# Kernel tuning notes

Measured on AMD Instinct MI355X. Metric: run time of the kernel, lower is better.

## Reference

```python
import jax, jax.numpy as jnp
import numpy as np

INPUT_SIZE = 256
NUM_LABELS = 50
L = NUM_LABELS + 1  # internal label count incl. pad label (index L-1)
B, T = 64, 256


def setup_inputs() -> dict:
    key = jax.random.key(0)
    k = jax.random.split(key, 8)
    inp = {
        "input": jax.random.normal(k[0], (B, T, INPUT_SIZE), dtype=jnp.float32),
        "mask": jnp.ones((B, T), dtype=jnp.float32),
        "target": jax.random.randint(k[1], (B, T), 0, NUM_LABELS),
        # state_nn: Linear(input_size, L)
        "state_W": jax.random.normal(k[2], (INPUT_SIZE, L), dtype=jnp.float32) * 0.05,
        "state_b": jnp.zeros((L,), dtype=jnp.float32),
        # trans_nn: Linear(input_size, L*L) (bigram=True)
        "trans_W": jax.random.normal(k[3], (INPUT_SIZE, L * L), dtype=jnp.float32) * 0.05,
        "trans_b": jnp.zeros((L * L,), dtype=jnp.float32),
    }
    return inp


def _energy(x, mask, state_W, state_b, trans_W, trans_b):
    # out_s: [B,T,L]  (unary scores), out_t: [B,T,L,L] (bigram transitions)
    out_s = jnp.einsum("bti,il->btl", x, state_W) + state_b
    out_t = (jnp.einsum("bti,io->bto", x, trans_W) + trans_b).reshape(
        x.shape[0], x.shape[1], L, L
    )
    energy = out_t + out_s[:, :, None, :]  # [B,T,L,L]
    return energy * mask[:, :, None, None]


def reference(input, mask, target, state_W, state_b, trans_W, trans_b):
    """ChainCRF.loss: -log p(target | input) per batch element, shape [B]."""
    energy = _energy(input, mask, state_W, state_b, trans_W, trans_b)
    e_t = jnp.transpose(energy, (1, 0, 2, 3))  # [T,B,L,L]
    tgt_t = target.T                            # [T,B]
    msk_t = mask.T                              # [T,B]
    bidx = jnp.arange(input.shape[0])

    # t = 0: start from pad label (index L-1)
    partition0 = e_t[0][:, L - 1, :]                       # [B,L]
    tgt0 = e_t[0][bidx, L - 1, tgt_t[0]]                   # [B]

    def step(carry, xs):
        part, tgt_e, prev = carry
        curr, tgt, m = xs  # curr [B,L,L], tgt [B], m [B]
        part_new = jax.nn.logsumexp(curr + part[:, :, None], axis=1)
        part = part + (part_new - part) * m[:, None]
        tgt_e = tgt_e + curr[bidx, prev, tgt]
        return (part, tgt_e, tgt), None

    (part, tgt_e, _), _ = jax.lax.scan(
        step, (partition0, tgt0, tgt_t[0]), (e_t[1:], tgt_t[1:], msk_t[1:])
    )
    return jax.nn.logsumexp(part, axis=1) - tgt_e
```

## Files before the change

kernel.cpp:

```cpp
#include <hip/hip_runtime.h>
#include <hip/hip_bf16.h>

#define B_    64
#define T_    256
#define K_    256
#define L_    51
#define LL_   2601
#define RS_   64
#define NG_   3328
#define PST_  4096
#define MT_   128
#define NT_   128
#define TS_   72

typedef __bf16 bf16x8 __attribute__((ext_vector_type(8)));
typedef float  f32x4  __attribute__((ext_vector_type(4)));
typedef unsigned int u32x4 __attribute__((ext_vector_type(4)));
typedef u32x4 __attribute__((may_alias)) u32x4_a;
typedef unsigned long long ull;
typedef ull __attribute__((may_alias)) ull_a;

static __device__ __forceinline__ bf16x8 as_bf16x8(u32x4 u) {
    return __builtin_bit_cast(bf16x8, u);
}
static __device__ __forceinline__ unsigned short bf16bits(float x) {
    return __builtin_bit_cast(unsigned short, __float2bfloat16(x));
}
static __device__ __forceinline__ ull pack4(f32x4 a) {
    return (ull)bf16bits(a[0]) | ((ull)bf16bits(a[1]) << 16) |
           ((ull)bf16bits(a[2]) << 32) | ((ull)bf16bits(a[3]) << 48);
}
static __device__ __forceinline__ void gld_lds16(const void* g, void* l) {
    __builtin_amdgcn_global_load_lds(
        (const __attribute__((address_space(1))) unsigned int*)g,
        (__attribute__((address_space(3))) unsigned int*)l, 16, 0, 0);
}

#define DPP_STEP(v, OP, CTRL)                                                   \
    {                                                                           \
        int _x = __builtin_bit_cast(int, v);                                    \
        float _o = __builtin_bit_cast(                                          \
            float, __builtin_amdgcn_update_dpp(_x, _x, CTRL, 0xF, 0xF, true));  \
        v = OP(v, _o);                                                          \
    }
static __device__ __forceinline__ float addf(float a, float b) { return a + b; }

__global__ __launch_bounds__(256) void prep_w(
    const float* __restrict__ trans_W, const float* __restrict__ trans_b,
    const float* __restrict__ state_W, const float* __restrict__ state_b,
    __hip_bfloat16* __restrict__ Wt, float* __restrict__ bias)
{
    const int n  = blockIdx.x * 64 + (threadIdx.x >> 2);
    const int kq = (threadIdx.x & 3) * 64;
    const int j  = n >> 6;
    const int i  = n & 63;
    const bool valid = (i < L_) && (j < L_);
    const int o = i * L_ + j;

    __hip_bfloat16 tmp[64];
#pragma unroll
    for (int kk = 0; kk < 64; ++kk) {
        const int k = kq + kk;
        float w = valid ? (trans_W[(size_t)k * LL_ + o] + state_W[k * L_ + j]) : 0.f;
        tmp[kk] = __float2bfloat16(w);
    }
    u32x4* dst = (u32x4*)(Wt + (size_t)n * K_ + kq);
    const u32x4* src = (const u32x4*)tmp;
#pragma unroll
    for (int q = 0; q < 8; ++q) dst[q] = src[q];

    if ((threadIdx.x & 3) == 0)
        bias[n] = valid ? (trans_b[o] + state_b[j]) : 0.f;
}

__global__ void prep_x(const float4* __restrict__ x4, ushort4* __restrict__ xb4, int n4)
{
    for (int idx = blockIdx.x * blockDim.x + threadIdx.x; idx < n4;
         idx += gridDim.x * blockDim.x) {
        float4 v = x4[idx];
        ushort4 o;
        o.x = bf16bits(v.x); o.y = bf16bits(v.y);
        o.z = bf16bits(v.z); o.w = bf16bits(v.w);
        xb4[idx] = o;
    }
}

__global__ void zero_pad(u32x4* __restrict__ P16, int nBT)
{
    const int per = (PST_ - NG_) / 8;
    const int tot = nBT * per;
    const u32x4 z = {};
    for (int idx = blockIdx.x * blockDim.x + threadIdx.x; idx < tot;
         idx += gridDim.x * blockDim.x) {
        const int m = idx / per;
        const int q = idx - m * per;
        P16[(size_t)m * (PST_ / 8) + (NG_ / 8) + q] = z;
    }
}

__global__ __launch_bounds__(256) void gemm_energy(
    const __hip_bfloat16* __restrict__ xb,
    const __hip_bfloat16* __restrict__ Wt,
    const float* __restrict__ bias,
    const float* __restrict__ mask,
    __hip_bfloat16* __restrict__ P,
    int t0, int Tc, int TcShift)
{
    __shared__ __align__(16) __hip_bfloat16 As[MT_ * 128];
    __shared__ __align__(16) __hip_bfloat16 Bs[NT_ * 128];

    const int tid  = threadIdx.x;
    const int lane = tid & 63;
    const int wv   = tid >> 6;
    const int quad = lane >> 4;
    const int l16  = lane & 15;
    const int m0 = blockIdx.y * MT_;
    const int n0 = blockIdx.x * NT_;
    const int mrow0 = (wv >> 1) * 64;
    const int ncol0 = (wv & 1) * 64;

    const int srow = wv * 4 + (lane >> 4);
    const int spos = lane & 15;

    f32x4 acc[4][4] = {};

    for (int kp = 0; kp < 2; ++kp) {
        if (kp) __syncthreads();
#pragma unroll
        for (int it = 0; it < 8; ++it) {
            const int r  = it * 16 + srow;
            const int kc = spos ^ (r & 15);
            const int ma = m0 + r;
            const int rg = (ma >> TcShift) * T_ + t0 + (ma & (Tc - 1));
            gld_lds16((const char*)xb + (size_t)rg * 512 + kp * 256 + kc * 16,
                      (char*)As + it * 4096 + wv * 1024);
            gld_lds16((const char*)Wt + (size_t)(n0 + r) * 512 + kp * 256 + kc * 16,
                      (char*)Bs + it * 4096 + wv * 1024);
        }
        asm volatile("s_waitcnt vmcnt(0)" ::: "memory");
        __syncthreads();

        const u32x4_a* Av = (const u32x4_a*)As;
        const u32x4_a* Bv = (const u32x4_a*)Bs;
#pragma unroll
        for (int kk = 0; kk < 4; ++kk) {
            bf16x8 af[4], bfr[4];
#pragma unroll
            for (int f = 0; f < 4; ++f) {
                const int ra = mrow0 + f * 16 + l16;
                af[f]  = as_bf16x8(Av[ra * 16 + ((kk * 4 + quad) ^ (ra & 15))]);
                const int rb = ncol0 + f * 16 + l16;
                bfr[f] = as_bf16x8(Bv[rb * 16 + ((kk * 4 + quad) ^ (rb & 15))]);
            }
#pragma unroll
            for (int nf = 0; nf < 4; ++nf)
#pragma unroll
                for (int mf = 0; mf < 4; ++mf)
                    acc[nf][mf] = __builtin_amdgcn_mfma_f32_16x16x32_bf16(
                        bfr[nf], af[mf], acc[nf][mf], 0, 0, 0);
        }
    }

    const int jcol = (n0 + ncol0) >> 6;
    const bool jok = jcol < L_;
#pragma unroll
    for (int mf = 0; mf < 4; ++mf) {
        const int m  = m0 + mrow0 + mf * 16 + l16;
        const int bb = m >> TcShift;
        const int tl = m & (Tc - 1);
        const int t  = t0 + tl;
        const float mval = mask[bb * T_ + t];
        const bool idm = (mval == 0.f) && (t != 0);
        __hip_bfloat16* prow = P + (size_t)m * PST_;
#pragma unroll
        for (int nf = 0; nf < 4; ++nf) {
            const int nbase = n0 + ncol0 + nf * 16 + quad * 4;
            const int ibase = nf * 16 + quad * 4;
            const f32x4 bv = *(const f32x4*)(bias + nbase);
            ull pk = 0;
#pragma unroll
            for (int r = 0; r < 4; ++r) {
                const int i = ibase + r;
                const bool ok = jok && (i < L_);
                float v;
                if (idm) v = (ok && i == jcol) ? 1.f : 0.f;
                else     v = ok ? __expf((acc[nf][mf][r] + bv[r]) * mval) : 0.f;
                pk |= (ull)bf16bits(v) << (16 * r);
            }
            *(ull_a*)(prow + nbase) = pk;
        }
    }
}

__global__ __launch_bounds__(256) void prod_quad(
    const __hip_bfloat16* __restrict__ P,
    __hip_bfloat16* __restrict__ Q,
    int Tc)
{
    __shared__ u32x4 Sm[4][512];
    __shared__ __align__(16) unsigned short T1t[64 * TS_];
    __shared__ __align__(16) unsigned short T3t[64 * TS_];
    __shared__ __align__(16) unsigned short W2t[64 * TS_];
    __shared__ __align__(16) unsigned short W4b[64 * TS_];

    const int tid  = threadIdx.x;
    const int wv   = tid >> 6;
    const int lane = tid & 63;
    const int quad = lane >> 4;
    const int l16  = lane & 15;
    const int bq = blockIdx.x;
    const int Tq = Tc >> 2;
    const int b  = bq / Tq;
    const int tq = bq - b * Tq;
    const __hip_bfloat16* tile0 = P + (size_t)(b * Tc + tq * 4) * PST_;

#pragma unroll
    for (int q = 0; q < 8; ++q) {
        const int idx  = q * 4 + wv;
        const int tile = idx >> 3;
        const int part = idx & 7;
        const int slot = part * 64 + lane;
        const int r    = slot >> 3;
        const int csrc = (slot & 7) ^ (r & 7);
        gld_lds16((const char*)(tile0 + (size_t)tile * PST_) + (r * 8 + csrc) * 16,
                  (char*)&Sm[tile][part * 64]);
    }

    u32x4 idf[2];
    {
        const int e = l16 & 7;
        const unsigned int bits = (e & 1) ? 0x3F800000u : 0x3F80u;
#pragma unroll
        for (int par = 0; par < 2; ++par) {
            u32x4 v = {};
            if (quad == (l16 >> 3) + par * 2) v[e >> 1] = bits;
            idf[par] = v;
        }
    }

    const int ra = wv * 16 + l16;
    const f32x4 z = {};
    asm volatile("s_waitcnt vmcnt(0)" ::: "memory");
    __syncthreads();

#pragma unroll
    for (int tt = 0; tt < 2; ++tt) {
        const u32x4* S = Sm[tt * 2];
        bf16x8 a0 = as_bf16x8(S[ra * 8 + (quad ^ (ra & 7))]);
        bf16x8 a1 = as_bf16x8(S[ra * 8 + ((4 + quad) ^ (ra & 7))]);
        unsigned short* dst = tt ? T3t : T1t;
#pragma unroll
        for (int nf = 0; nf < 4; ++nf) {
            f32x4 d = __builtin_amdgcn_mfma_f32_16x16x32_bf16(
                (nf >> 1) ? a1 : a0, as_bf16x8(idf[nf & 1]), z, 0, 0, 0);
            *(ull_a*)(dst + (nf * 16 + l16) * TS_ + wv * 16 + quad * 4) = pack4(d);
        }
    }
    __syncthreads();

    {
        bf16x8 a2[2], a3[2];
#pragma unroll
        for (int ks = 0; ks < 2; ++ks) {
            a2[ks] = as_bf16x8(Sm[1][ra * 8 + ((ks * 4 + quad) ^ (ra & 7))]);
            a3[ks] = as_bf16x8(*(const u32x4_a*)(T3t + ra * TS_ + ks * 32 + quad * 8));
        }
#pragma unroll
        for (int nf = 0; nf < 4; ++nf) {
            const int rb = nf * 16 + l16;
            f32x4 u = z, v = z;
#pragma unroll
            for (int ks = 0; ks < 2; ++ks) {
                bf16x8 bU = as_bf16x8(*(const u32x4_a*)(T1t + rb * TS_ + ks * 32 + quad * 8));
                bf16x8 bV = as_bf16x8(Sm[3][rb * 8 + ((ks * 4 + quad) ^ (rb & 7))]);
                u = __builtin_amdgcn_mfma_f32_16x16x32_bf16(a2[ks], bU, u, 0, 0, 0);
                v = __builtin_amdgcn_mfma_f32_16x16x32_bf16(a3[ks], bV, v, 0, 0, 0);
            }
            *(ull_a*)(W2t + rb * TS_ + wv * 16 + quad * 4) = pack4(u);
            *(ull_a*)(W4b + rb * TS_ + wv * 16 + quad * 4) = pack4(v);
        }
    }
    __syncthreads();

    {
        bf16x8 aw[2];
#pragma unroll
        for (int ks = 0; ks < 2; ++ks)
            aw[ks] = as_bf16x8(*(const u32x4_a*)(W2t + ra * TS_ + ks * 32 + quad * 8));
#pragma unroll
        for (int nf = 0; nf < 4; ++nf) {
            const int rb = nf * 16 + l16;
            f32x4 d = z;
#pragma unroll
            for (int ks = 0; ks < 2; ++ks) {
                bf16x8 bw = as_bf16x8(*(const u32x4_a*)(W4b + rb * TS_ + ks * 32 + quad * 8));
                d = __builtin_amdgcn_mfma_f32_16x16x32_bf16(aw[ks], bw, d, 0, 0, 0);
            }
            *(ull_a*)(T1t + rb * TS_ + wv * 16 + quad * 4) = pack4(d);
        }
    }
    __syncthreads();

    u32x4* qout = (u32x4*)(Q + (size_t)bq * PST_);
#pragma unroll
    for (int c = tid; c < 512; c += 256) {
        const int row = c >> 3;
        const int pos = c & 7;
        qout[row * 8 + pos] = *(const u32x4_a*)(T1t + row * TS_ + pos * 8);
    }
}

__global__ __launch_bounds__(64) void tgt_kernel(
    const __hip_bfloat16* __restrict__ P, const int* __restrict__ target,
    const float* __restrict__ mask, float* __restrict__ tgt_ws, int t0, int Tc)
{
    const int b = blockIdx.x, lane = threadIdx.x;
    float s = 0.f;
    for (int tl = lane; tl < Tc; tl += 64) {
        const int t = t0 + tl;
        const int j = target[b * T_ + t];
        const int i = (t == 0) ? (L_ - 1) : target[b * T_ + t - 1];
        const float m = (t == 0) ? 1.f : mask[b * T_ + t];
        if (m != 0.f) {
            const float pval = __bfloat162float(P[(size_t)(b * Tc + tl) * PST_ + j * RS_ + i]);
            s += __logf(pval);
        }
    }
#pragma unroll
    for (int d = 1; d < 64; d <<= 1) s += __shfl_xor(s, d);
    if (lane == 0) {
        if (t0 == 0) tgt_ws[b] = s;
        else         tgt_ws[b] += s;
    }
}

__global__ __launch_bounds__(64, 1) void scan_q(
    const __hip_bfloat16* __restrict__ Q,
    float* __restrict__ p_ws, float* __restrict__ ls_ws,
    const float* __restrict__ tgt_ws, float* __restrict__ out,
    int t0q, int Tq, int Tqtot)
{
    __shared__ __align__(16) unsigned short p_arr[64];

    const int b    = blockIdx.x;
    const int lane = threadIdx.x;
    const int quad = lane >> 4;
    const int l16  = lane & 15;

    float pv[4] = {0.f, 0.f, 0.f, 0.f};
    float logscale = 0.f;
    if (t0q == 0) {
        p_arr[lane] = (lane == L_ - 1) ? (unsigned short)0x3F80 : (unsigned short)0;
    } else {
#pragma unroll
        for (int f = 0; f < 4; ++f) pv[f] = p_ws[b * 64 + f * 16 + l16];
        logscale = ls_ws[b];
        p_arr[quad * 16 + l16] = bf16bits(pv[quad]);
    }
    asm volatile("s_waitcnt lgkmcnt(0)" ::: "memory");

    int off[8];
#pragma unroll
    for (int f = 0; f < 4; ++f)
#pragma unroll
        for (int ks = 0; ks < 2; ++ks)
            off[f * 2 + ks] = (f * 16 + l16) * 8 + ks * 4 + quad;

    const u32x4* gp = (const u32x4*)Q + (size_t)b * Tq * (PST_ / 8);
    const u32x4_a* pa = (const u32x4_a*)p_arr;

    u32x4 s0[8], s1[8], s2[8], s3[8];
    auto fetch = [&](u32x4 (&st)[8], int tl) {
        const u32x4* g = gp + (size_t)tl * (PST_ / 8);
#pragma unroll
        for (int q = 0; q < 8; ++q) st[q] = g[off[q]];
    };
    fetch(s0, 0);
    if (1 < Tq) fetch(s1, 1);
    if (2 < Tq) fetch(s2, 2);
    if (3 < Tq) fetch(s3, 3);

    auto step = [&](u32x4 (&st)[8], int tl) {
        bf16x8 a0 = as_bf16x8(pa[quad]);
        bf16x8 a1 = as_bf16x8(pa[4 + quad]);
        const f32x4 z = {};
        f32x4 ae[4], ao[4];
#pragma unroll
        for (int f = 0; f < 4; ++f) {
            ae[f] = __builtin_amdgcn_mfma_f32_16x16x32_bf16(a0, as_bf16x8(st[f * 2 + 0]), z, 0, 0, 0);
            ao[f] = __builtin_amdgcn_mfma_f32_16x16x32_bf16(a1, as_bf16x8(st[f * 2 + 1]), z, 0, 0, 0);
        }
#pragma unroll
        for (int f = 0; f < 4; ++f) pv[f] = ae[f][0] + ao[f][0];

        if (((tl & 1) == 1) || (tl == Tq - 1)) {
            float mx = fmaxf(fmaxf(pv[0], pv[1]), fmaxf(pv[2], pv[3]));
            DPP_STEP(mx, fmaxf, 0xB1);
            DPP_STEP(mx, fmaxf, 0x4E);
            DPP_STEP(mx, fmaxf, 0x124);
            DPP_STEP(mx, fmaxf, 0x128);
            const float inv = 1.f / mx;
            logscale += __logf(mx);
#pragma unroll
            for (int f = 0; f < 4; ++f) pv[f] *= inv;
        }
        p_arr[quad * 16 + l16] = bf16bits(pv[quad]);
        asm volatile("s_waitcnt lgkmcnt(0)" ::: "memory");
    };

    for (int tl = 0; tl < Tq; tl += 4) {
        step(s0, tl);
        if (tl + 4 < Tq) fetch(s0, tl + 4);
        if (tl + 1 < Tq) { step(s1, tl + 1); if (tl + 5 < Tq) fetch(s1, tl + 5); }
        if (tl + 2 < Tq) { step(s2, tl + 2); if (tl + 6 < Tq) fetch(s2, tl + 6); }
        if (tl + 3 < Tq) { step(s3, tl + 3); if (tl + 7 < Tq) fetch(s3, tl + 7); }
    }

    if (t0q + Tq == Tqtot) {
        float s = pv[0] + pv[1] + pv[2] + pv[3];
        DPP_STEP(s, addf, 0xB1);
        DPP_STEP(s, addf, 0x4E);
        DPP_STEP(s, addf, 0x124);
        DPP_STEP(s, addf, 0x128);
        if (lane == 0) out[b] = logscale + __logf(s) - tgt_ws[b];
    } else {
        if (quad == 0) {
#pragma unroll
            for (int f = 0; f < 4; ++f) p_ws[b * 64 + f * 16 + l16] = pv[f];
        }
        if (lane == 0) ls_ws[b] = logscale;
    }
}

extern "C" void kernel_launch(void* const* d_in, const int* in_sizes, int n_in,
                              void* d_out, int out_size, void* d_ws, size_t ws_size,
                              hipStream_t stream)
{
    (void)in_sizes; (void)n_in; (void)out_size;
    const float* x       = (const float*)d_in[0];
    const float* mask    = (const float*)d_in[1];
    const int*   target  = (const int*)d_in[2];
    const float* state_W = (const float*)d_in[3];
    const float* state_b = (const float*)d_in[4];
    const float* trans_W = (const float*)d_in[5];
    const float* trans_b = (const float*)d_in[6];
    float* out = (float*)d_out;

    char* ws = (char*)d_ws;
    size_t off = 0;
    auto alloc = [&](size_t bytes) -> void* {
        void* p = ws + off;
        off = (off + bytes + 255) & ~(size_t)255;
        return p;
    };

    __hip_bfloat16* Wt   = (__hip_bfloat16*)alloc((size_t)NG_ * K_ * 2);
    float*          bias = (float*)alloc((size_t)NG_ * 4);
    __hip_bfloat16* xb   = (__hip_bfloat16*)alloc((size_t)B_ * T_ * K_ * 2);
    float*          p_ws = (float*)alloc((size_t)B_ * 64 * 4);
    float*          ls   = (float*)alloc((size_t)B_ * 4);
    float*          tgte = (float*)alloc((size_t)B_ * 4);
    const size_t fixed = off;

    int Tc = 256;
    while (Tc > 4 && fixed + (size_t)Tc * B_ * PST_ * 2 * 5 / 4 + 512 > ws_size) Tc >>= 1;
    __hip_bfloat16* P = (__hip_bfloat16*)alloc((size_t)Tc * B_ * PST_ * 2);
    __hip_bfloat16* Q = (__hip_bfloat16*)alloc((size_t)(Tc / 4) * B_ * PST_ * 2);
    int TcShift = 0;
    while ((1 << TcShift) < Tc) ++TcShift;

    prep_w<<<dim3(NG_ / 64), 256, 0, stream>>>(trans_W, trans_b, state_W, state_b, Wt, bias);
    prep_x<<<dim3(2048), 256, 0, stream>>>((const float4*)x, (ushort4*)xb, B_ * T_ * K_ / 4);
    zero_pad<<<dim3(2048), 256, 0, stream>>>((u32x4*)P, B_ * Tc);

    for (int t0 = 0; t0 < T_; t0 += Tc) {
        gemm_energy<<<dim3(NG_ / NT_, (B_ * Tc) / MT_), 256, 0, stream>>>(
            xb, Wt, bias, mask, P, t0, Tc, TcShift);
        prod_quad<<<dim3(B_ * (Tc / 4)), 256, 0, stream>>>(P, Q, Tc);
        tgt_kernel<<<dim3(B_), 64, 0, stream>>>(P, target, mask, tgte, t0, Tc);
        scan_q<<<dim3(B_), 64, 0, stream>>>(Q, p_ws, ls, tgte, out,
                                            t0 / 4, Tc / 4, T_ / 4);
    }
}
```

Baseline: 229.8 us.

## Fuse prep kernels, stage GEMM epilogue through LDS, merge target into scan

Merges the weight-transpose, x-to-bf16 conversion and pad-zeroing kernels into one launch, and rewrites the weight transpose to go through shared memory so global accesses are coalesced. The GEMM epilogue now writes its bf16 tile to LDS first, then stores full 16-byte rows to P instead of scattered 8-byte writes. The target-score kernel is folded into scan_q as a second wave that runs alongside the scan. Together these remove launches and uncoalesced traffic, at the cost of an extra LDS round trip and two extra barriers in the GEMM.

After: 213.9 us. 6.9% less time.

```diff
diff --git a/kernel.cpp b/kernel.cpp
--- a/kernel.cpp
+++ b/kernel.cpp
@@ -12,6 +12,7 @@
 #define MT_   128
 #define NT_   128
 #define TS_   72
+#define ES_   136
 
 typedef __bf16 bf16x8 __attribute__((ext_vector_type(8)));
 typedef float  f32x4  __attribute__((ext_vector_type(4)));
@@ -45,56 +46,70 @@
     }
 static __device__ __forceinline__ float addf(float a, float b) { return a + b; }
 
-__global__ __launch_bounds__(256) void prep_w(
+__global__ __launch_bounds__(256) void prep_all(
     const float* __restrict__ trans_W, const float* __restrict__ trans_b,
     const float* __restrict__ state_W, const float* __restrict__ state_b,
-    __hip_bfloat16* __restrict__ Wt, float* __restrict__ bias)
+    const float* __restrict__ x,
+    __hip_bfloat16* __restrict__ Wt, float* __restrict__ bias,
+    __hip_bfloat16* __restrict__ xb, __hip_bfloat16* __restrict__ P, int Tc)
 {
-    const int n  = blockIdx.x * 64 + (threadIdx.x >> 2);
-    const int kq = (threadIdx.x & 3) * 64;
-    const int j  = n >> 6;
-    const int i  = n & 63;
-    const bool valid = (i < L_) && (j < L_);
-    const int o = i * L_ + j;
-
-    __hip_bfloat16 tmp[64];
-#pragma unroll
-    for (int kk = 0; kk < 64; ++kk) {
-        const int k = kq + kk;
-        float w = valid ? (trans_W[(size_t)k * LL_ + o] + state_W[k * L_ + j]) : 0.f;
-        tmp[kk] = __float2bfloat16(w);
-    }
-    u32x4* dst = (u32x4*)(Wt + (size_t)n * K_ + kq);
-    const u32x4* src = (const u32x4*)tmp;
-#pragma unroll
-    for (int q = 0; q < 8; ++q) dst[q] = src[q];
-
-    if ((threadIdx.x & 3) == 0)
-        bias[n] = valid ? (trans_b[o] + state_b[j]) : 0.f;
-}
-
-__global__ void prep_x(const float4* __restrict__ x4, ushort4* __restrict__ xb4, int n4)
-{
-    for (int idx = blockIdx.x * blockDim.x + threadIdx.x; idx < n4;
-         idx += gridDim.x * blockDim.x) {
-        float4 v = x4[idx];
-        ushort4 o;
-        o.x = bf16bits(v.x); o.y = bf16bits(v.y);
-        o.z = bf16bits(v.z); o.w = bf16bits(v.w);
-        xb4[idx] = o;
-    }
-}
-
-__global__ void zero_pad(u32x4* __restrict__ P16, int nBT)
-{
-    const int per = (PST_ - NG_) / 8;
-    const int tot = nBT * per;
-    const u32x4 z = {};
-    for (int idx = blockIdx.x * blockDim.x + threadIdx.x; idx < tot;
-         idx += gridDim.x * blockDim.x) {
-        const int m = idx / per;
-        const int q = idx - m * per;
-        P16[(size_t)m * (PST_ / 8) + (NG_ / 8) + q] = z;
+    __shared__ __align__(16) __hip_bfloat16 Wl[52 * 258];
+    const int blk = blockIdx.x, tid = threadIdx.x;
+
+    if (blk < 64) {
+        const int i = blk;
+        if (i < L_) {
+            const int jp = tid & 63, kk = tid >> 6;
+            if (jp < 52) {
+                for (int k = kk; k < K_; k += 4) {
+                    float v = 0.f;
+                    if (jp < L_) v = trans_W[(size_t)k * LL_ + i * L_ + jp] +
+                                     state_W[k * L_ + jp];
+                    Wl[jp * 258 + k] = __float2bfloat16(v);
+                }
+            }
+            __syncthreads();
+            for (int idx = tid; idx < 52 * 32; idx += 256) {
+                const int j = idx >> 5, c = idx & 31;
+                const unsigned int* row = (const unsigned int*)&Wl[j * 258];
+                u32x4 v;
+                v[0] = row[c * 4 + 0]; v[1] = row[c * 4 + 1];
+                v[2] = row[c * 4 + 2]; v[3] = row[c * 4 + 3];
+                *(u32x4*)(Wt + (size_t)((j << 6) + i) * K_ + c * 8) = v;
+            }
+        } else {
+            const u32x4 z = {};
+            for (int idx = tid; idx < 52 * 32; idx += 256) {
+                const int j = idx >> 5, c = idx & 31;
+                *(u32x4*)(Wt + (size_t)((j << 6) + i) * K_ + c * 8) = z;
+            }
+        }
+        if (tid < 52) {
+            const int j = tid;
+            bias[(j << 6) + i] =
+                (i < L_ && j < L_) ? trans_b[i * L_ + j] + state_b[j] : 0.f;
+        }
+    } else if (blk < 64 + 1024) {
+        const int n4 = B_ * T_ * K_ / 4;
+        const float4* x4 = (const float4*)x;
+        ushort4* xb4 = (ushort4*)xb;
+        for (int idx = (blk - 64) * 256 + tid; idx < n4; idx += 1024 * 256) {
+            float4 v = x4[idx];
+            ushort4 o;
+            o.x = bf16bits(v.x); o.y = bf16bits(v.y);
+            o.z = bf16bits(v.z); o.w = bf16bits(v.w);
+            xb4[idx] = o;
+        }
+    } else {
+        const int per = (PST_ - NG_) / 8;
+        const int tot = B_ * Tc * per;
+        u32x4* P16 = (u32x4*)P;
+        const u32x4 z = {};
+        for (int idx = (blk - 1088) * 256 + tid; idx < tot; idx += 1024 * 256) {
+            const int m = idx / per;
+            const int q = idx - m * per;
+            P16[(size_t)m * (PST_ / 8) + (NG_ / 8) + q] = z;
+        }
     }
 }
 
@@ -106,8 +121,9 @@
     __hip_bfloat16* __restrict__ P,
     int t0, int Tc, int TcShift)
 {
-    __shared__ __align__(16) __hip_bfloat16 As[MT_ * 128];
-    __shared__ __align__(16) __hip_bfloat16 Bs[NT_ * 128];
+    __shared__ __align__(16) __hip_bfloat16 SH[2 * MT_ * 128];
+    __hip_bfloat16* As = SH;
+    __hip_bfloat16* Bs = SH + MT_ * 128;
 
     const int tid  = threadIdx.x;
     const int lane = tid & 63;
@@ -160,35 +176,45 @@
                         bfr[nf], af[mf], acc[nf][mf], 0, 0, 0);
         }
     }
-
+    __syncthreads();
+
+    unsigned short* E = (unsigned short*)SH;
     const int jcol = (n0 + ncol0) >> 6;
     const bool jok = jcol < L_;
 #pragma unroll
     for (int mf = 0; mf < 4; ++mf) {
-        const int m  = m0 + mrow0 + mf * 16 + l16;
+        const int ml = mrow0 + mf * 16 + l16;
+        const int m  = m0 + ml;
         const int bb = m >> TcShift;
         const int tl = m & (Tc - 1);
         const int t  = t0 + tl;
         const float mval = mask[bb * T_ + t];
         const bool idm = (mval == 0.f) && (t != 0);
-        __hip_bfloat16* prow = P + (size_t)m * PST_;
 #pragma unroll
         for (int nf = 0; nf < 4; ++nf) {
-            const int nbase = n0 + ncol0 + nf * 16 + quad * 4;
-            const int ibase = nf * 16 + quad * 4;
-            const f32x4 bv = *(const f32x4*)(bias + nbase);
+            const int nl = ncol0 + nf * 16 + quad * 4;
+            const f32x4 bv = *(const f32x4*)(bias + n0 + nl);
             ull pk = 0;
 #pragma unroll
             for (int r = 0; r < 4; ++r) {
-                const int i = ibase + r;
+                const int i = (nl + r) & 63;
                 const bool ok = jok && (i < L_);
                 float v;
                 if (idm) v = (ok && i == jcol) ? 1.f : 0.f;
                 else     v = ok ? __expf((acc[nf][mf][r] + bv[r]) * mval) : 0.f;
                 pk |= (ull)bf16bits(v) << (16 * r);
             }
-            *(ull_a*)(prow + nbase) = pk;
-        }
+            *(ull_a*)(E + ml * ES_ + nl) = pk;
+        }
+    }
+    __syncthreads();
+
+#pragma unroll
+    for (int it2 = 0; it2 < 8; ++it2) {
+        const int idx = it2 * 256 + tid;
+        const int ml = idx >> 4, c = idx & 15;
+        const u32x4 v = *(const u32x4_a*)(E + ml * ES_ + c * 8);
+        *(u32x4*)(P + (size_t)(m0 + ml) * PST_ + n0 + c * 8) = v;
     }
 }
 
@@ -310,125 +336,133 @@
     }
 }
 
-__global__ __launch_bounds__(64) void tgt_kernel(
-    const __hip_bfloat16* __restrict__ P, const int* __restrict__ target,
-    const float* __restrict__ mask, float* __restrict__ tgt_ws, int t0, int Tc)
-{
-    const int b = blockIdx.x, lane = threadIdx.x;
-    float s = 0.f;
-    for (int tl = lane; tl < Tc; tl += 64) {
-        const int t = t0 + tl;
-        const int j = target[b * T_ + t];
-        const int i = (t == 0) ? (L_ - 1) : target[b * T_ + t - 1];
-        const float m = (t == 0) ? 1.f : mask[b * T_ + t];
-        if (m != 0.f) {
-            const float pval = __bfloat162float(P[(size_t)(b * Tc + tl) * PST_ + j * RS_ + i]);
-            s += __logf(pval);
-        }
-    }
-#pragma unroll
-    for (int d = 1; d < 64; d <<= 1) s += __shfl_xor(s, d);
-    if (lane == 0) {
-        if (t0 == 0) tgt_ws[b] = s;
-        else         tgt_ws[b] += s;
-    }
-}
-
-__global__ __launch_bounds__(64, 1) void scan_q(
+__global__ __launch_bounds__(128, 1) void scan_q(
     const __hip_bfloat16* __restrict__ Q,
+    const __hip_bfloat16* __restrict__ P,
+    const int* __restrict__ target, const float* __restrict__ mask,
     float* __restrict__ p_ws, float* __restrict__ ls_ws,
-    const float* __restrict__ tgt_ws, float* __restrict__ out,
+    float* __restrict__ tgt_ws, float* __restrict__ out,
     int t0q, int Tq, int Tqtot)
 {
     __shared__ __align__(16) unsigned short p_arr[64];
+    __shared__ float tgt_sh;
 
     const int b    = blockIdx.x;
-    const int lane = threadIdx.x;
+    const int tid  = threadIdx.x;
+    const int wv   = tid >> 6;
+    const int lane = tid & 63;
     const int quad = lane >> 4;
     const int l16  = lane & 15;
+    const int t0 = t0q << 2, Tc = Tq << 2;
 
     float pv[4] = {0.f, 0.f, 0.f, 0.f};
     float logscale = 0.f;
-    if (t0q == 0) {
-        p_arr[lane] = (lane == L_ - 1) ? (unsigned short)0x3F80 : (unsigned short)0;
+
+    if (wv == 0) {
+        if (t0q == 0) {
+            p_arr[lane] = (lane == L_ - 1) ? (unsigned short)0x3F80 : (unsigned short)0;
+        } else {
+#pragma unroll
+            for (int f = 0; f < 4; ++f) pv[f] = p_ws[b * 64 + f * 16 + l16];
+            logscale = ls_ws[b];
+            p_arr[quad * 16 + l16] = bf16bits(pv[quad]);
+        }
+        asm volatile("s_waitcnt lgkmcnt(0)" ::: "memory");
+
+        int off[8];
+#pragma unroll
+        for (int f = 0; f < 4; ++f)
+#pragma unroll
+            for (int ks = 0; ks < 2; ++ks)
+                off[f * 2 + ks] = (f * 16 + l16) * 8 + ks * 4 + quad;
+
+        const u32x4* gp = (const u32x4*)Q + (size_t)b * Tq * (PST_ / 8);
+        const u32x4_a* pa = (const u32x4_a*)p_arr;
+
+        u32x4 s0[8], s1[8], s2[8], s3[8];
+        auto fetch = [&](u32x4 (&st)[8], int tl) {
+            const u32x4* g = gp + (size_t)tl * (PST_ / 8);
+#pragma unroll
+            for (int q = 0; q < 8; ++q) st[q] = g[off[q]];
+        };
+        fetch(s0, 0);
+        if (1 < Tq) fetch(s1, 1);
+        if (2 < Tq) fetch(s2, 2);
+        if (3 < Tq) fetch(s3, 3);
+
+        auto step = [&](u32x4 (&st)[8], int tl) {
+            bf16x8 a0 = as_bf16x8(pa[quad]);
+            bf16x8 a1 = as_bf16x8(pa[4 + quad]);
+            const f32x4 z = {};
+            f32x4 ae[4], ao[4];
+#pragma unroll
+            for (int f = 0; f < 4; ++f) {
+                ae[f] = __builtin_amdgcn_mfma_f32_16x16x32_bf16(a0, as_bf16x8(st[f * 2 + 0]), z, 0, 0, 0);
+                ao[f] = __builtin_amdgcn_mfma_f32_16x16x32_bf16(a1, as_bf16x8(st[f * 2 + 1]), z, 0, 0, 0);
+            }
+#pragma unroll
+            for (int f = 0; f < 4; ++f) pv[f] = ae[f][0] + ao[f][0];
+
+            if (((tl & 1) == 1) || (tl == Tq - 1)) {
+                float mx = fmaxf(fmaxf(pv[0], pv[1]), fmaxf(pv[2], pv[3]));
+                DPP_STEP(mx, fmaxf, 0xB1);
+                DPP_STEP(mx, fmaxf, 0x4E);
+                DPP_STEP(mx, fmaxf, 0x124);
+                DPP_STEP(mx, fmaxf, 0x128);
+                const float inv = 1.f / mx;
+                logscale += __logf(mx);
+#pragma unroll
+                for (int f = 0; f < 4; ++f) pv[f] *= inv;
+            }
+            p_arr[quad * 16 + l16] = bf16bits(pv[quad]);
+            asm volatile("s_waitcnt lgkmcnt(0)" ::: "memory");
+        };
+
+        for (int tl = 0; tl < Tq; tl += 4) {
+            step(s0, tl);
+            if (tl + 4 < Tq) fetch(s0, tl + 4);
+            if (tl + 1 < Tq) { step(s1, tl + 1); if (tl + 5 < Tq) fetch(s1, tl + 5); }
+            if (tl + 2 < Tq) { step(s2, tl + 2); if (tl + 6 < Tq) fetch(s2, tl + 6); }
+            if (tl + 3 < Tq) { step(s3, tl + 3); if (tl + 7 < Tq) fetch(s3, tl + 7); }
+        }
     } else {
-#pragma unroll
-        for (int f = 0; f < 4; ++f) pv[f] = p_ws[b * 64 + f * 16 + l16];
-        logscale = ls_ws[b];
-        p_arr[quad * 16 + l16] = bf16bits(pv[quad]);
-    }
-    asm volatile("s_waitcnt lgkmcnt(0)" ::: "memory");
-
-    int off[8];
-#pragma unroll
-    for (int f = 0; f < 4; ++f)
-#pragma unroll
-        for (int ks = 0; ks < 2; ++ks)
-            off[f * 2 + ks] = (f * 16 + l16) * 8 + ks * 4 + quad;
-
-    const u32x4* gp = (const u32x4*)Q + (size_t)b * Tq * (PST_ / 8);
-    const u32x4_a* pa = (const u32x4_a*)p_arr;
-
-    u32x4 s0[8], s1[8], s2[8], s3[8];
-    auto fetch = [&](u32x4 (&st)[8], int tl) {
-        const u32x4* g = gp + (size_t)tl * (PST_ / 8);
-#pragma unroll
-        for (int q = 0; q < 8; ++q) st[q] = g[off[q]];
-    };
-    fetch(s0, 0);
-    if (1 < Tq) fetch(s1, 1);
-    if (2 < Tq) fetch(s2, 2);
-    if (3 < Tq) fetch(s3, 3);
-
-    auto step = [&](u32x4 (&st)[8], int tl) {
-        bf16x8 a0 = as_bf16x8(pa[quad]);
-        bf16x8 a1 = as_bf16x8(pa[4 + quad]);
-        const f32x4 z = {};
-        f32x4 ae[4], ao[4];
-#pragma unroll
-        for (int f = 0; f < 4; ++f) {
-            ae[f] = __builtin_amdgcn_mfma_f32_16x16x32_bf16(a0, as_bf16x8(st[f * 2 + 0]), z, 0, 0, 0);
-            ao[f] = __builtin_amdgcn_mfma_f32_16x16x32_bf16(a1, as_bf16x8(st[f * 2 + 1]), z, 0, 0, 0);
-        }
-#pragma unroll
-        for (int f = 0; f < 4; ++f) pv[f] = ae[f][0] + ao[f][0];
-
-        if (((tl & 1) == 1) || (tl == Tq - 1)) {
-            float mx = fmaxf(fmaxf(pv[0], pv[1]), fmaxf(pv[2], pv[3]));
-            DPP_STEP(mx, fmaxf, 0xB1);
-            DPP_STEP(mx, fmaxf, 0x4E);
-            DPP_STEP(mx, fmaxf, 0x124);
-            DPP_STEP(mx, fmaxf, 0x128);
-            const float inv = 1.f / mx;
-            logscale += __logf(mx);
-#pragma unroll
-            for (int f = 0; f < 4; ++f) pv[f] *= inv;
-        }
-        p_arr[quad * 16 + l16] = bf16bits(pv[quad]);
-        asm volatile("s_waitcnt lgkmcnt(0)" ::: "memory");
-    };
-
-    for (int tl = 0; tl < Tq; tl += 4) {
-        step(s0, tl);
-        if (tl + 4 < Tq) fetch(s0, tl + 4);
-        if (tl + 1 < Tq) { step(s1, tl + 1); if (tl + 5 < Tq) fetch(s1, tl + 5); }
-        if (tl + 2 < Tq) { step(s2, tl + 2); if (tl + 6 < Tq) fetch(s2, tl + 6); }
-        if (tl + 3 < Tq) { step(s3, tl + 3); if (tl + 7 < Tq) fetch(s3, tl + 7); }
-    }
-
-    if (t0q + Tq == Tqtot) {
-        float s = pv[0] + pv[1] + pv[2] + pv[3];
-        DPP_STEP(s, addf, 0xB1);
-        DPP_STEP(s, addf, 0x4E);
-        DPP_STEP(s, addf, 0x124);
-        DPP_STEP(s, addf, 0x128);
-        if (lane == 0) out[b] = logscale + __logf(s) - tgt_ws[b];
-    } else {
-        if (quad == 0) {
-#pragma unroll
-            for (int f = 0; f < 4; ++f) p_ws[b * 64 + f * 16 + l16] = pv[f];
-        }
-        if (lane == 0) ls_ws[b] = logscale;
+        float s = 0.f;
+        for (int tl = lane; tl < Tc; tl += 64) {
+            const int t = t0 + tl;
+            const int j = target[b * T_ + t];
+            const int i = (t == 0) ? (L_ - 1) : target[b * T_ + t - 1];
+            const float m = (t == 0) ? 1.f : mask[b * T_ + t];
+            if (m != 0.f) {
+                const float pval =
+                    __bfloat162float(P[(size_t)(b * Tc + tl) * PST_ + j * RS_ + i]);
+                s += __logf(pval);
+            }
+        }
+#pragma unroll
+        for (int d = 1; d < 64; d <<= 1) s += __shfl_xor(s, d);
+        if (lane == 0) {
+            const float tot = (t0 == 0) ? s : tgt_ws[b] + s;
+            tgt_ws[b] = tot;
+            tgt_sh = tot;
+        }
+    }
+    __syncthreads();
+
+    if (wv == 0) {
+        if (t0q + Tq == Tqtot) {
+            float s = pv[0] + pv[1] + pv[2] + pv[3];
+            DPP_STEP(s, addf, 0xB1);
+            DPP_STEP(s, addf, 0x4E);
+            DPP_STEP(s, addf, 0x124);
+            DPP_STEP(s, addf, 0x128);
+            if (lane == 0) out[b] = logscale + __logf(s) - tgt_sh;
+        } else {
+            if (quad == 0) {
+#pragma unroll
+                for (int f = 0; f < 4; ++f) p_ws[b * 64 + f * 16 + l16] = pv[f];
+            }
+            if (lane == 0) ls_ws[b] = logscale;
+        }
     }
 }
 
@@ -469,16 +503,14 @@
     int TcShift = 0;
     while ((1 << TcShift) < Tc) ++TcShift;
 
-    prep_w<<<dim3(NG_ / 64), 256, 0, stream>>>(trans_W, trans_b, state_W, state_b, Wt, bias);
-    prep_x<<<dim3(2048), 256, 0, stream>>>((const float4*)x, (ushort4*)xb, B_ * T_ * K_ / 4);
-    zero_pad<<<dim3(2048), 256, 0, stream>>>((u32x4*)P, B_ * Tc);
+    prep_all<<<dim3(2112), 256, 0, stream>>>(
+        trans_W, trans_b, state_W, state_b, x, Wt, bias, xb, P, Tc);
 
     for (int t0 = 0; t0 < T_; t0 += Tc) {
         gemm_energy<<<dim3(NG_ / NT_, (B_ * Tc) / MT_), 256, 0, stream>>>(
             xb, Wt, bias, mask, P, t0, Tc, TcShift);
         prod_quad<<<dim3(B_ * (Tc / 4)), 256, 0, stream>>>(P, Q, Tc);
-        tgt_kernel<<<dim3(B_), 64, 0, stream>>>(P, target, mask, tgte, t0, Tc);
-        scan_q<<<dim3(B_), 64, 0, stream>>>(Q, p_ws, ls, tgte, out,
-                                            t0 / 4, Tc / 4, T_ / 4);
-    }
-}
+        scan_q<<<dim3(B_), 128, 0, stream>>>(Q, P, target, mask, p_ws, ls, tgte, out,
+                                             t0 / 4, Tc / 4, T_ / 4);
+    }
+}
```
